# Optimization experiments

Measured on AMD Instinct MI355X. Metric: run time of the kernel, lower is better.

The kernel has to match this reference:

```python
import jax, jax.numpy as jnp
import numpy as np
from jax import lax

B, C_IN, H, W = 64, 64, 36, 36
N_UNITS = 2048


def setup_inputs() -> dict:
    key = jax.random.key(0)
    k1, k2, k3, k4 = jax.random.split(key, 4)
    x = jax.random.normal(k1, (B, C_IN, H, W), dtype=jnp.float32)
    feat_weights = jax.random.normal(k2, (N_UNITS, C_IN, 1, 1), dtype=jnp.float32) * 0.1
    biases = jax.random.normal(k3, (N_UNITS,), dtype=jnp.float32)
    space_weights = jax.random.normal(k4, (N_UNITS, H, W), dtype=jnp.float32) * 0.05
    return {"x": x, "feat_weights": feat_weights, "biases": biases,
            "space_weights": space_weights}


def reference(x, feat_weights, biases, space_weights):
    # 1x1 channel-mixing conv: [B,Cin,H,W] x [U,Cin] -> [B,U,H,W]
    feat = jnp.einsum('bchw,uc->buhw', x, feat_weights[:, :, 0, 0])
    # grouped (depthwise, groups=n_units) valid conv; kernel spans full spatial
    # extent, so output is [B, U, 1, 1]
    space = lax.conv_general_dilated(
        feat, space_weights[:, None, :, :],
        window_strides=(1, 1), padding='VALID',
        feature_group_count=N_UNITS,
        dimension_numbers=('NCHW', 'OIHW', 'NCHW'))
    out = space + biases[None, :, None, None]
    return out
```

## Files before the change

kernel.cpp:

```cpp
#include <hip/hip_runtime.h>
#include <hip/hip_bf16.h>
#include <stdint.h>

#define NB 64
#define NC 64
#define NU 2048
#define K_REAL 1296
#define K_PAD  1344
#define M_ROWS 4096

#define BM 256
#define BN 128
#define NKS 42

typedef __attribute__((ext_vector_type(4))) float f32x4;
typedef __attribute__((ext_vector_type(8))) short bf16x8;

__device__ __forceinline__ unsigned short f2bf_rne(float f) {
  union { float f; uint32_t u; } v; v.f = f;
  uint32_t u = v.u;
  return (unsigned short)((u + 0x7FFFu + ((u >> 16) & 1u)) >> 16);
}

__global__ void convert_pad_kernel(const float* __restrict__ x,
                                   const float* __restrict__ sw,
                                   unsigned short* __restrict__ dst) {
  const int KB = K_PAD / 8;
  const int total = (M_ROWS + NU) * KB;
  for (int idx = blockIdx.x * blockDim.x + threadIdx.x; idx < total;
       idx += gridDim.x * blockDim.x) {
    int r  = idx / KB;
    int kb = idx - r * KB;
    int k0 = kb * 8;
    uint32_t p0 = 0, p1 = 0, p2 = 0, p3 = 0;
    if (k0 + 8 <= K_REAL) {
      const float* srow = (r < M_ROWS) ? (x + (size_t)r * K_REAL)
                                       : (sw + (size_t)(r - M_ROWS) * K_REAL);
      const float4* s = (const float4*)(srow + k0);
      float4 f0 = s[0];
      float4 f1 = s[1];
      p0 = (uint32_t)f2bf_rne(f0.x) | ((uint32_t)f2bf_rne(f0.y) << 16);
      p1 = (uint32_t)f2bf_rne(f0.z) | ((uint32_t)f2bf_rne(f0.w) << 16);
      p2 = (uint32_t)f2bf_rne(f1.x) | ((uint32_t)f2bf_rne(f1.y) << 16);
      p3 = (uint32_t)f2bf_rne(f1.z) | ((uint32_t)f2bf_rne(f1.w) << 16);
    }
    uint4 o; o.x = p0; o.y = p1; o.z = p2; o.w = p3;
    *(uint4*)(dst + (size_t)r * K_PAD + k0) = o;
  }
}

__global__ __launch_bounds__(512, 1)
void fused_readout_gemm(const unsigned short* __restrict__ Abf,
                        const unsigned short* __restrict__ Bbf,
                        const float* __restrict__ fw,
                        const float* __restrict__ bias,
                        float* __restrict__ out) {
  __shared__ unsigned short As[5][8192];
  __shared__ unsigned short Bs[5][4096];

  const int tid  = threadIdx.x;
  const int lane = tid & 63;
  const int w    = tid >> 6;
  const int wm   = w >> 1;
  const int wn   = w & 1;
  const int g    = lane >> 4;
  const int rl   = lane & 15;

  const int braw  = (int)blockIdx.x;
  const int xcd   = braw & 7;
  const int idx   = braw >> 3;
  const int tileM = (xcd >> 1) * 4 + (idx & 3);
  const int tileN = (xcd & 1) * 8 + (idx >> 2);
  const int rowA0 = tileM * BM;
  const int colB0 = tileN * BN;

  const int lc  = tid ^ ((tid >> 3) & 3);
  const int sr  = lc >> 2;
  const int sc  = lc & 3;
  const unsigned short* srcA = Abf + (size_t)(rowA0 + sr) * K_PAD + sc * 8;
  const unsigned short* srcB = Bbf + (size_t)(colB0 + sr) * K_PAD + sc * 8;

  const int laneOff = rl * 64 + ((g * 16) ^ (((rl >> 1) & 3) << 4));

#define GLOAD(dst, src)                                                         \
  __builtin_amdgcn_global_load_lds(                                             \
      (const __attribute__((address_space(1))) unsigned int*)(const void*)(src),\
      (__attribute__((address_space(3))) unsigned int*)(void*)(dst), 16, 0, 0)

#define SLOT(j, koff)                                                           \
  do {                                                                          \
    char* _pa = (char*)&As[j][0];                                               \
    GLOAD(_pa + tid * 16, srcA + (koff));                                       \
    GLOAD(_pa + 8192 + tid * 16, srcA + (size_t)128 * K_PAD + (koff));          \
    GLOAD((char*)&Bs[j][0] + tid * 16, srcB + (koff));                          \
  } while (0)

#define LDFRAGS(j)                                                              \
  do {                                                                          \
    const char* _pa = (const char*)&As[j][0] + wm * 4096 + laneOff;             \
    av[0] = *(const bf16x8*)(_pa);                                              \
    av[1] = *(const bf16x8*)(_pa + 1024);                                       \
    av[2] = *(const bf16x8*)(_pa + 2048);                                       \
    av[3] = *(const bf16x8*)(_pa + 3072);                                       \
    const char* _pb = (const char*)&Bs[j][0] + wn * 4096 + laneOff;             \
    bv[0] = *(const bf16x8*)(_pb);                                              \
    bv[1] = *(const bf16x8*)(_pb + 1024);                                       \
    bv[2] = *(const bf16x8*)(_pb + 2048);                                       \
    bv[3] = *(const bf16x8*)(_pb + 3072);                                       \
  } while (0)

#define MFMA16()                                                                \
  do {                                                                          \
    __builtin_amdgcn_s_setprio(1);                                              \
    _Pragma("unroll") for (int _m = 0; _m < 4; ++_m)                            \
      _Pragma("unroll") for (int _n = 0; _n < 4; ++_n)                          \
        acc[_m][_n] = __builtin_amdgcn_mfma_f32_16x16x32_bf16(                  \
            av[_m], bv[_n], acc[_m][_n], 0, 0, 0);                              \
    __builtin_amdgcn_s_setprio(0);                                              \
  } while (0)

#define BAR()                                                                   \
  do { __builtin_amdgcn_s_barrier(); __builtin_amdgcn_sched_barrier(0); } while (0)
#define VMW(N)                                                                  \
  do { asm volatile("s_waitcnt vmcnt(" #N ")" ::: "memory");                    \
       __builtin_amdgcn_sched_barrier(0); } while (0)

  f32x4 acc[4][4];
#pragma unroll
  for (int m = 0; m < 4; ++m)
#pragma unroll
    for (int n = 0; n < 4; ++n) acc[m][n] = (f32x4)0.f;

  bf16x8 av[4], bv[4];

  SLOT(0, 0); SLOT(1, 32); SLOT(2, 64); SLOT(3, 96);
  VMW(9); BAR();

  int kb = 128;
#pragma unroll 1
  for (int it = 0; it < 7; ++it) {
    LDFRAGS(0); SLOT(4, kb);       BAR(); MFMA16(); VMW(9); BAR();
    LDFRAGS(1); SLOT(0, kb + 32);  BAR(); MFMA16(); VMW(9); BAR();
    LDFRAGS(2); SLOT(1, kb + 64);  BAR(); MFMA16(); VMW(9); BAR();
    LDFRAGS(3); SLOT(2, kb + 96);  BAR(); MFMA16(); VMW(9); BAR();
    LDFRAGS(4); SLOT(3, kb + 128); BAR(); MFMA16(); VMW(9); BAR();
    kb += 160;
  }
  LDFRAGS(0); SLOT(4, 1248); BAR(); MFMA16(); VMW(9); BAR();
  LDFRAGS(1); SLOT(0, 1280); BAR(); MFMA16(); VMW(9); BAR();
  LDFRAGS(2); SLOT(1, 1312); BAR(); MFMA16(); VMW(9); BAR();
  LDFRAGS(3);                BAR(); MFMA16(); VMW(6); BAR();
  LDFRAGS(4);                BAR(); MFMA16(); VMW(3); BAR();
  LDFRAGS(0);                BAR(); MFMA16(); VMW(0); BAR();
  LDFRAGS(1);                BAR(); MFMA16();

#undef GLOAD
#undef SLOT
#undef LDFRAGS
#undef MFMA16
#undef BAR
#undef VMW

  const int bidx = tileM * 4 + wm;
  float vtmp[4];
#pragma unroll
  for (int n = 0; n < 4; ++n) {
    const int u = colB0 + wn * 64 + n * 16 + rl;
    const float* fwrow = fw + (size_t)u * NC;
    float s = 0.f;
#pragma unroll
    for (int m = 0; m < 4; ++m) {
      float4 w4 = *(const float4*)(fwrow + m * 16 + g * 4);
      f32x4 a_ = acc[m][n];
      s += w4.x * a_[0] + w4.y * a_[1] + w4.z * a_[2] + w4.w * a_[3];
    }
    s += __shfl_xor(s, 16, 64);
    s += __shfl_xor(s, 32, 64);
    vtmp[n] = s;
  }
  const int ucol = colB0 + wn * 64 + lane;
  float r = (g == 0) ? vtmp[0] : (g == 1) ? vtmp[1] : (g == 2) ? vtmp[2] : vtmp[3];
  out[(size_t)bidx * NU + ucol] = r + bias[ucol];
}

extern "C" void kernel_launch(void* const* d_in, const int* in_sizes, int n_in,
                              void* d_out, int out_size, void* d_ws, size_t ws_size,
                              hipStream_t stream) {
  const float* x    = (const float*)d_in[0];
  const float* fw   = (const float*)d_in[1];
  const float* bias = (const float*)d_in[2];
  const float* sw   = (const float*)d_in[3];
  float* out = (float*)d_out;

  unsigned short* Abf = (unsigned short*)d_ws;
  unsigned short* Bbf = Abf + (size_t)M_ROWS * K_PAD;

  {
    int total = (M_ROWS + NU) * (K_PAD / 8);
    int blocks = (total + 255) / 256;
    if (blocks > 2048) blocks = 2048;
    convert_pad_kernel<<<blocks, 256, 0, stream>>>(x, sw, Abf);
  }

  fused_readout_gemm<<<dim3(256), 512, 0, stream>>>(Abf, Bbf, fw, bias, out);
}
```

Before: 42.24 us.

## Restructure GEMM pipeline to 3-stage buffer with 64-wide K steps

Replaces the 5-slot, 32-wide-K LDS ring with a 3-stage ring whose slots each hold two 32-wide K halves. Each step now runs two rounds of 16 MFMAs, which halves the number of barrier pairs per unit of K. The second half's fragments load after the barrier, overlapping with the first half's MFMAs. In exchange the prefetch distance shrinks to two slots of 64 K and more registers are held for the doubled fragment sets. LDS use stays about the same.

```diff
diff --git a/kernel.cpp b/kernel.cpp
--- a/kernel.cpp
+++ b/kernel.cpp
@@ -11,7 +11,6 @@
 
 #define BM 256
 #define BN 128
-#define NKS 42
 
 typedef __attribute__((ext_vector_type(4))) float f32x4;
 typedef __attribute__((ext_vector_type(8))) short bf16x8;
@@ -55,8 +54,8 @@
                         const float* __restrict__ fw,
                         const float* __restrict__ bias,
                         float* __restrict__ out) {
-  __shared__ unsigned short As[5][8192];
-  __shared__ unsigned short Bs[5][4096];
+  __shared__ unsigned short As[3][2][8192];
+  __shared__ unsigned short Bs[3][2][4096];
 
   const int tid  = threadIdx.x;
   const int lane = tid & 63;
@@ -89,33 +88,37 @@
 
 #define SLOT(j, koff)                                                           \
   do {                                                                          \
-    char* _pa = (char*)&As[j][0];                                               \
-    GLOAD(_pa + tid * 16, srcA + (koff));                                       \
-    GLOAD(_pa + 8192 + tid * 16, srcA + (size_t)128 * K_PAD + (koff));          \
-    GLOAD((char*)&Bs[j][0] + tid * 16, srcB + (koff));                          \
+    char* _pa0 = (char*)&As[j][0][0];                                           \
+    GLOAD(_pa0 + tid * 16, srcA + (koff));                                      \
+    GLOAD(_pa0 + 8192 + tid * 16, srcA + (size_t)128 * K_PAD + (koff));         \
+    char* _pa1 = (char*)&As[j][1][0];                                           \
+    GLOAD(_pa1 + tid * 16, srcA + (koff) + 32);                                 \
+    GLOAD(_pa1 + 8192 + tid * 16, srcA + (size_t)128 * K_PAD + (koff) + 32);    \
+    GLOAD((char*)&Bs[j][0][0] + tid * 16, srcB + (koff));                       \
+    GLOAD((char*)&Bs[j][1][0] + tid * 16, srcB + (koff) + 32);                  \
   } while (0)
 
-#define LDFRAGS(j)                                                              \
+#define LDF(j, h, AV, BV)                                                       \
   do {                                                                          \
-    const char* _pa = (const char*)&As[j][0] + wm * 4096 + laneOff;             \
-    av[0] = *(const bf16x8*)(_pa);                                              \
-    av[1] = *(const bf16x8*)(_pa + 1024);                                       \
-    av[2] = *(const bf16x8*)(_pa + 2048);                                       \
-    av[3] = *(const bf16x8*)(_pa + 3072);                                       \
-    const char* _pb = (const char*)&Bs[j][0] + wn * 4096 + laneOff;             \
-    bv[0] = *(const bf16x8*)(_pb);                                              \
-    bv[1] = *(const bf16x8*)(_pb + 1024);                                       \
-    bv[2] = *(const bf16x8*)(_pb + 2048);                                       \
-    bv[3] = *(const bf16x8*)(_pb + 3072);                                       \
+    const char* _pa = (const char*)&As[j][h][0] + wm * 4096 + laneOff;          \
+    AV[0] = *(const bf16x8*)(_pa);                                              \
+    AV[1] = *(const bf16x8*)(_pa + 1024);                                       \
+    AV[2] = *(const bf16x8*)(_pa + 2048);                                       \
+    AV[3] = *(const bf16x8*)(_pa + 3072);                                       \
+    const char* _pb = (const char*)&Bs[j][h][0] + wn * 4096 + laneOff;          \
+    BV[0] = *(const bf16x8*)(_pb);                                              \
+    BV[1] = *(const bf16x8*)(_pb + 1024);                                       \
+    BV[2] = *(const bf16x8*)(_pb + 2048);                                       \
+    BV[3] = *(const bf16x8*)(_pb + 3072);                                       \
   } while (0)
 
-#define MFMA16()                                                                \
+#define MFMA16(AV, BV)                                                          \
   do {                                                                          \
     __builtin_amdgcn_s_setprio(1);                                              \
     _Pragma("unroll") for (int _m = 0; _m < 4; ++_m)                            \
       _Pragma("unroll") for (int _n = 0; _n < 4; ++_n)                          \
         acc[_m][_n] = __builtin_amdgcn_mfma_f32_16x16x32_bf16(                  \
-            av[_m], bv[_n], acc[_m][_n], 0, 0, 0);                              \
+            AV[_m], BV[_n], acc[_m][_n], 0, 0, 0);                              \
     __builtin_amdgcn_s_setprio(0);                                              \
   } while (0)
 
@@ -131,32 +134,32 @@
 #pragma unroll
     for (int n = 0; n < 4; ++n) acc[m][n] = (f32x4)0.f;
 
-  bf16x8 av[4], bv[4];
-
-  SLOT(0, 0); SLOT(1, 32); SLOT(2, 64); SLOT(3, 96);
-  VMW(9); BAR();
-
-  int kb = 128;
+  bf16x8 av0[4], bv0[4], av1[4], bv1[4];
+
+  SLOT(0, 0); SLOT(1, 64);
+  VMW(6); BAR();
+
+  int kb = 0;
 #pragma unroll 1
-  for (int it = 0; it < 7; ++it) {
-    LDFRAGS(0); SLOT(4, kb);       BAR(); MFMA16(); VMW(9); BAR();
-    LDFRAGS(1); SLOT(0, kb + 32);  BAR(); MFMA16(); VMW(9); BAR();
-    LDFRAGS(2); SLOT(1, kb + 64);  BAR(); MFMA16(); VMW(9); BAR();
-    LDFRAGS(3); SLOT(2, kb + 96);  BAR(); MFMA16(); VMW(9); BAR();
-    LDFRAGS(4); SLOT(3, kb + 128); BAR(); MFMA16(); VMW(9); BAR();
-    kb += 160;
-  }
-  LDFRAGS(0); SLOT(4, 1248); BAR(); MFMA16(); VMW(9); BAR();
-  LDFRAGS(1); SLOT(0, 1280); BAR(); MFMA16(); VMW(9); BAR();
-  LDFRAGS(2); SLOT(1, 1312); BAR(); MFMA16(); VMW(9); BAR();
-  LDFRAGS(3);                BAR(); MFMA16(); VMW(6); BAR();
-  LDFRAGS(4);                BAR(); MFMA16(); VMW(3); BAR();
-  LDFRAGS(0);                BAR(); MFMA16(); VMW(0); BAR();
-  LDFRAGS(1);                BAR(); MFMA16();
+  for (int it = 0; it < 6; ++it) {
+    SLOT(2, kb + 128); LDF(0, 0, av0, bv0); BAR(); LDF(0, 1, av1, bv1);
+    MFMA16(av0, bv0); MFMA16(av1, bv1); VMW(6); BAR();
+    SLOT(0, kb + 192); LDF(1, 0, av0, bv0); BAR(); LDF(1, 1, av1, bv1);
+    MFMA16(av0, bv0); MFMA16(av1, bv1); VMW(6); BAR();
+    SLOT(1, kb + 256); LDF(2, 0, av0, bv0); BAR(); LDF(2, 1, av1, bv1);
+    MFMA16(av0, bv0); MFMA16(av1, bv1); VMW(6); BAR();
+    kb += 192;
+  }
+  SLOT(2, 1280); LDF(0, 0, av0, bv0); BAR(); LDF(0, 1, av1, bv1);
+  MFMA16(av0, bv0); MFMA16(av1, bv1); VMW(6); BAR();
+  LDF(1, 0, av0, bv0); BAR(); LDF(1, 1, av1, bv1);
+  MFMA16(av0, bv0); MFMA16(av1, bv1); VMW(0); BAR();
+  LDF(2, 0, av0, bv0); BAR(); LDF(2, 1, av1, bv1);
+  MFMA16(av0, bv0); MFMA16(av1, bv1);
 
 #undef GLOAD
 #undef SLOT
-#undef LDFRAGS
+#undef LDF
 #undef MFMA16
 #undef BAR
 #undef VMW
```

Result: slower. 45.50 us (+7.7%).

## Split GEMM reduction dimension in two and add combine kernel

Applied to the files above, without the earlier changes.

Splits the K dimension of the bf16 GEMM into two halves, doubling the grid to 512 blocks so every CU gets work. Each block writes a partial epilogue result to a workspace buffer. A new combine kernel then sums the two partials and adds the bias. The LDS pipeline shrinks from 5 stages to 3 and launch bounds are raised so more blocks can be resident, at the cost of an extra launch and a round trip of the partials through global memory.

```diff
diff --git a/kernel.cpp b/kernel.cpp
--- a/kernel.cpp
+++ b/kernel.cpp
@@ -8,10 +8,10 @@
 #define K_REAL 1296
 #define K_PAD  1344
 #define M_ROWS 4096
+#define K_SPLIT 672
 
 #define BM 256
 #define BN 128
-#define NKS 42
 
 typedef __attribute__((ext_vector_type(4))) float f32x4;
 typedef __attribute__((ext_vector_type(8))) short bf16x8;
@@ -49,14 +49,13 @@
   }
 }
 
-__global__ __launch_bounds__(512, 1)
+__global__ __launch_bounds__(512, 4)
 void fused_readout_gemm(const unsigned short* __restrict__ Abf,
                         const unsigned short* __restrict__ Bbf,
                         const float* __restrict__ fw,
-                        const float* __restrict__ bias,
-                        float* __restrict__ out) {
-  __shared__ unsigned short As[5][8192];
-  __shared__ unsigned short Bs[5][4096];
+                        float* __restrict__ part) {
+  __shared__ unsigned short As[3][8192];
+  __shared__ unsigned short Bs[3][4096];
 
   const int tid  = threadIdx.x;
   const int lane = tid & 63;
@@ -69,16 +68,18 @@
   const int braw  = (int)blockIdx.x;
   const int xcd   = braw & 7;
   const int idx   = braw >> 3;
-  const int tileM = (xcd >> 1) * 4 + (idx & 3);
-  const int tileN = (xcd & 1) * 8 + (idx >> 2);
+  const int split = xcd >> 2;
+  const int tileM = (xcd & 3) * 4 + (idx & 3);
+  const int tileN = idx >> 2;
   const int rowA0 = tileM * BM;
   const int colB0 = tileN * BN;
+  const int kS    = split * K_SPLIT;
 
   const int lc  = tid ^ ((tid >> 3) & 3);
   const int sr  = lc >> 2;
   const int sc  = lc & 3;
-  const unsigned short* srcA = Abf + (size_t)(rowA0 + sr) * K_PAD + sc * 8;
-  const unsigned short* srcB = Bbf + (size_t)(colB0 + sr) * K_PAD + sc * 8;
+  const unsigned short* srcA = Abf + (size_t)(rowA0 + sr) * K_PAD + kS + sc * 8;
+  const unsigned short* srcB = Bbf + (size_t)(colB0 + sr) * K_PAD + kS + sc * 8;
 
   const int laneOff = rl * 64 + ((g * 16) ^ (((rl >> 1) & 3) << 4));
 
@@ -133,26 +134,20 @@
 
   bf16x8 av[4], bv[4];
 
-  SLOT(0, 0); SLOT(1, 32); SLOT(2, 64); SLOT(3, 96);
-  VMW(9); BAR();
-
-  int kb = 128;
+  SLOT(0, 0); SLOT(1, 32);
+  VMW(3); BAR();
+
+  int kb = 64;
 #pragma unroll 1
-  for (int it = 0; it < 7; ++it) {
-    LDFRAGS(0); SLOT(4, kb);       BAR(); MFMA16(); VMW(9); BAR();
-    LDFRAGS(1); SLOT(0, kb + 32);  BAR(); MFMA16(); VMW(9); BAR();
-    LDFRAGS(2); SLOT(1, kb + 64);  BAR(); MFMA16(); VMW(9); BAR();
-    LDFRAGS(3); SLOT(2, kb + 96);  BAR(); MFMA16(); VMW(9); BAR();
-    LDFRAGS(4); SLOT(3, kb + 128); BAR(); MFMA16(); VMW(9); BAR();
-    kb += 160;
-  }
-  LDFRAGS(0); SLOT(4, 1248); BAR(); MFMA16(); VMW(9); BAR();
-  LDFRAGS(1); SLOT(0, 1280); BAR(); MFMA16(); VMW(9); BAR();
-  LDFRAGS(2); SLOT(1, 1312); BAR(); MFMA16(); VMW(9); BAR();
-  LDFRAGS(3);                BAR(); MFMA16(); VMW(6); BAR();
-  LDFRAGS(4);                BAR(); MFMA16(); VMW(3); BAR();
-  LDFRAGS(0);                BAR(); MFMA16(); VMW(0); BAR();
-  LDFRAGS(1);                BAR(); MFMA16();
+  for (int it = 0; it < 6; ++it) {
+    SLOT(2, kb);      LDFRAGS(0); BAR(); MFMA16(); VMW(3); BAR();
+    SLOT(0, kb + 32); LDFRAGS(1); BAR(); MFMA16(); VMW(3); BAR();
+    SLOT(1, kb + 64); LDFRAGS(2); BAR(); MFMA16(); VMW(3); BAR();
+    kb += 96;
+  }
+  SLOT(2, 640); LDFRAGS(0); BAR(); MFMA16(); VMW(3); BAR();
+  LDFRAGS(1);               BAR(); MFMA16(); VMW(0); BAR();
+  LDFRAGS(2);               BAR(); MFMA16();
 
 #undef GLOAD
 #undef SLOT
@@ -180,7 +175,26 @@
   }
   const int ucol = colB0 + wn * 64 + lane;
   float r = (g == 0) ? vtmp[0] : (g == 1) ? vtmp[1] : (g == 2) ? vtmp[2] : vtmp[3];
-  out[(size_t)bidx * NU + ucol] = r + bias[ucol];
+  part[((size_t)split * NB + bidx) * NU + ucol] = r;
+}
+
+__global__ __launch_bounds__(256)
+void combine_kernel(const float* __restrict__ part,
+                    const float* __restrict__ bias,
+                    float* __restrict__ out) {
+  int f = blockIdx.x * blockDim.x + threadIdx.x;
+  const float4* p0 = (const float4*)part;
+  const float4* p1 = (const float4*)(part + (size_t)NB * NU);
+  const float4* bz = (const float4*)bias;
+  float4 a = p0[f];
+  float4 b = p1[f];
+  float4 c = bz[f & 511];
+  float4 o;
+  o.x = a.x + b.x + c.x;
+  o.y = a.y + b.y + c.y;
+  o.z = a.z + b.z + c.z;
+  o.w = a.w + b.w + c.w;
+  ((float4*)out)[f] = o;
 }
 
 extern "C" void kernel_launch(void* const* d_in, const int* in_sizes, int n_in,
@@ -194,6 +208,7 @@
 
   unsigned short* Abf = (unsigned short*)d_ws;
   unsigned short* Bbf = Abf + (size_t)M_ROWS * K_PAD;
+  float* part = (float*)(Bbf + (size_t)NU * K_PAD);
 
   {
     int total = (M_ROWS + NU) * (K_PAD / 8);
@@ -202,5 +217,7 @@
     convert_pad_kernel<<<blocks, 256, 0, stream>>>(x, sw, Abf);
   }
 
-  fused_readout_gemm<<<dim3(256), 512, 0, stream>>>(Abf, Bbf, fw, bias, out);
-}
+  fused_readout_gemm<<<dim3(512), 512, 0, stream>>>(Abf, Bbf, fw, part);
+
+  combine_kernel<<<dim3((NB * NU / 4) / 256), 256, 0, stream>>>(part, bias, out);
+}
```

Result: slower. 44.45 us (+5.2%).
